# Optimization experiments

Hardware: AMD Instinct MI355X
Metric: run time of the kernel (lower is better)

The kernel has to match this reference:

```python
import jax, jax.numpy as jnp
import numpy as np

D_MODEL = 2048
N_HEADS = 16
D_HEAD = D_MODEL // N_HEADS
SQLEN = 2048
EPS = 1e-5
XPOS_SCALE_BASE = 512.0


def apply_xpos(x, offset, inv=False):
    # x: (sqlen, d_head). Rotary embedding with xPos exponential length scaling.
    sqlen, d = x.shape
    half = d // 2
    freq = 1.0 / (10000.0 ** (jnp.arange(half, dtype=jnp.float32) / half))
    pos = jnp.arange(sqlen, dtype=jnp.float32) + offset  # absolute positions
    ang = pos[:, None] * freq[None, :]                   # (sqlen, half)
    sin, cos = jnp.sin(ang), jnp.cos(ang)
    # xPos per-dim scale zeta^(pos/scale_base); k gets the inverse scale.
    zeta = (jnp.arange(half, dtype=jnp.float32) * 2.0 + 0.4 * d) / (1.4 * d)
    sc = zeta[None, :] ** (pos[:, None] / XPOS_SCALE_BASE)
    if inv:
        sc = 1.0 / sc
    x1, x2 = x[:, :half], x[:, half:]
    r1 = (x1 * cos - x2 * sin) * sc
    r2 = (x2 * cos + x1 * sin) * sc
    return jnp.concatenate([r1, r2], axis=-1)


def group_norm(x, weight, bias):
    # x: (sqlen, d_model); n_heads groups of d_head channels each.
    xg = x.reshape(x.shape[0], N_HEADS, D_HEAD)
    mu = jnp.mean(xg, axis=-1, keepdims=True)
    var = jnp.mean((xg - mu) ** 2, axis=-1, keepdims=True)
    xn = ((xg - mu) * jax.lax.rsqrt(var + EPS)).reshape(x.shape)
    return xn * weight + bias


def setup_inputs() -> dict:
    key = jax.random.key(0)
    ks = jax.random.split(key, 9)
    s = 0.02
    return {
        "x": jax.random.normal(ks[0], (SQLEN, D_MODEL), dtype=jnp.float32),
        "state": jax.random.normal(ks[1], (N_HEADS, D_HEAD, D_HEAD), dtype=jnp.float32),
        "W_qkv": jax.random.normal(ks[2], (3 * D_MODEL, D_MODEL), dtype=jnp.float32) * s,
        "W_alpha": jax.random.normal(ks[3], (N_HEADS, D_MODEL), dtype=jnp.float32) * s,
        "b_alpha": jnp.zeros((N_HEADS,), dtype=jnp.float32),
        "alpha_base": jnp.log(jax.random.uniform(ks[4], (N_HEADS,), minval=0.95, maxval=0.999)).astype(jnp.float32),
        "gn_weight": jnp.ones((D_MODEL,), dtype=jnp.float32),
        "gn_bias": jnp.zeros((D_MODEL,), dtype=jnp.float32),
        "W_out": jax.random.normal(ks[5], (D_MODEL, D_MODEL), dtype=jnp.float32) * s,
        "W_gate": jax.random.normal(ks[6], (D_MODEL, D_MODEL), dtype=jnp.float32) * s,
        "offset": 0,
    }


def reference(x, state, W_qkv, W_alpha, b_alpha, alpha_base, gn_weight, gn_bias, W_out, W_gate, offset):
    sqlen = x.shape[0]
    # qkv projection -> (3, h, sqlen, d_head)
    qkv = (x @ W_qkv.T).reshape(sqlen, 3, N_HEADS, D_HEAD).transpose(1, 2, 0, 3)
    q, k, v = qkv[0], qkv[1], qkv[2]
    q = jax.vmap(lambda t: apply_xpos(t, offset))(q)
    k = jax.vmap(lambda t: apply_xpos(t, offset, inv=True))(k)

    # per-head, per-position decay log-rates: (h, sqlen), negative
    alphas = jax.nn.sigmoid(x @ W_alpha.T + b_alpha).T
    alphas = alpha_base[:, None] * 8.0 * alphas
    k = (1.0 - jnp.exp(alphas))[:, :, None] * k
    alphas = jnp.cumsum(alphas, axis=1)
    # causal decay matrix Delta[h,i,j] = exp(a_i - a_j) for j <= i
    Delta = jnp.tril(jnp.exp(alphas[:, :, None] - alphas[:, None, :]))

    attn = jnp.einsum('hid,hjd,hij->hij', q, k, Delta)
    ret = jnp.einsum('hij,hje->ihe', attn, v)  # (sqlen, h, d_head)

    # recurrent state carry
    new_state = jnp.exp(alphas[:, -1, None, None]) * state
    ret = ret + jnp.einsum('hid,hde,hi->ihe', q, state, jnp.exp(alphas))
    new_state = new_state + jnp.einsum('hid,hie,hi->hde', k, v, Delta[:, -1, :])

    ret = ret.reshape(sqlen, D_MODEL)
    ret = group_norm(ret, gn_weight, gn_bias)
    out = (jax.nn.swish(ret @ W_gate.T) * ret) @ W_out.T
    return (out, new_state)
```

## Files before the change

### kernel.cpp

```cpp
#include <hip/hip_runtime.h>
#include <cstddef>

#define SQLEN 2048
#define DMODEL 2048
#define NHEADS 16
#define DHEAD 128

typedef __attribute__((ext_vector_type(8))) short bf16x8;
typedef __attribute__((ext_vector_type(4))) float floatx4;

__device__ __forceinline__ unsigned short f2bf(float f) {
  union { float f; unsigned u; } c; c.f = f;
  unsigned u = c.u;
  unsigned r = u + 0x7fffu + ((u >> 16) & 1u);
  return (unsigned short)(r >> 16);
}
__device__ __forceinline__ float bf2f(unsigned short s) {
  union { unsigned u; float f; } c; c.u = ((unsigned)s) << 16;
  return c.f;
}

__global__ __launch_bounds__(256) void f2b_kernel(const float4* __restrict__ in,
                                                  ushort4* __restrict__ out) {
  int i = blockIdx.x * 256 + threadIdx.x;
  float4 v = in[i];
  ushort4 o;
  o.x = f2bf(v.x); o.y = f2bf(v.y); o.z = f2bf(v.z); o.w = f2bf(v.w);
  out[i] = o;
}

__global__ __launch_bounds__(256) void f2b2_kernel(const float4* __restrict__ in0,
                                                   ushort4* __restrict__ out0,
                                                   const float4* __restrict__ in1,
                                                   ushort4* __restrict__ out1,
                                                   int half_blocks) {
  int b = blockIdx.x;
  const float4* in = (b < half_blocks) ? in0 : in1;
  ushort4* out = (b < half_blocks) ? out0 : out1;
  int i = (b < half_blocks ? b : b - half_blocks) * 256 + threadIdx.x;
  float4 v = in[i];
  ushort4 o;
  o.x = f2bf(v.x); o.y = f2bf(v.y); o.z = f2bf(v.z); o.w = f2bf(v.w);
  out[i] = o;
}

__global__ __launch_bounds__(256) void gemm_bf16_nt(const unsigned short* __restrict__ A,
                                                    const unsigned short* __restrict__ B,
                                                    float* __restrict__ C,
                                                    int M, int N, int K) {
  __shared__ __align__(16) unsigned short As[128 * 32];
  __shared__ __align__(16) unsigned short Bs[128 * 32];
  int tid = threadIdx.x;
  int wave = tid >> 6;
  int lane = tid & 63;
  int wm = wave >> 1, wn = wave & 1;
  int quad = lane >> 4, m16 = lane & 15;
  int row0 = blockIdx.y * 128, col0 = blockIdx.x * 128;

  floatx4 acc[4][4];
#pragma unroll
  for (int i = 0; i < 4; i++)
#pragma unroll
    for (int j = 0; j < 4; j++) acc[i][j] = (floatx4){0.f, 0.f, 0.f, 0.f};

  int c0 = tid, c1 = tid + 256;
  int r0c = c0 >> 2, q0c = (c0 & 3) * 8;
  int r1c = c1 >> 2, q1c = (c1 & 3) * 8;

  const size_t sK = (size_t)K;
  for (int k0 = 0; k0 < K; k0 += 32) {
    __builtin_amdgcn_global_load_lds(
        (const __attribute__((address_space(1))) unsigned int*)(A + (size_t)(row0 + r0c) * sK + k0 + q0c),
        (__attribute__((address_space(3))) unsigned int*)(As + c0 * 8), 16, 0, 0);
    __builtin_amdgcn_global_load_lds(
        (const __attribute__((address_space(1))) unsigned int*)(A + (size_t)(row0 + r1c) * sK + k0 + q1c),
        (__attribute__((address_space(3))) unsigned int*)(As + c1 * 8), 16, 0, 0);
    __builtin_amdgcn_global_load_lds(
        (const __attribute__((address_space(1))) unsigned int*)(B + (size_t)(col0 + r0c) * sK + k0 + q0c),
        (__attribute__((address_space(3))) unsigned int*)(Bs + c0 * 8), 16, 0, 0);
    __builtin_amdgcn_global_load_lds(
        (const __attribute__((address_space(1))) unsigned int*)(B + (size_t)(col0 + r1c) * sK + k0 + q1c),
        (__attribute__((address_space(3))) unsigned int*)(Bs + c1 * 8), 16, 0, 0);
    __syncthreads();

    bf16x8 af[4], bfr[4];
#pragma unroll
    for (int i = 0; i < 4; i++)
      af[i] = *(const bf16x8*)(As + (wm * 64 + i * 16 + m16) * 32 + quad * 8);
#pragma unroll
    for (int j = 0; j < 4; j++)
      bfr[j] = *(const bf16x8*)(Bs + (wn * 64 + j * 16 + m16) * 32 + quad * 8);
#pragma unroll
    for (int i = 0; i < 4; i++)
#pragma unroll
      for (int j = 0; j < 4; j++)
        acc[i][j] = __builtin_amdgcn_mfma_f32_16x16x32_bf16(af[i], bfr[j], acc[i][j], 0, 0, 0);
    __syncthreads();
  }

#pragma unroll
  for (int i = 0; i < 4; i++) {
#pragma unroll
    for (int j = 0; j < 4; j++) {
      int rr = row0 + wm * 64 + i * 16 + quad * 4;
      int cc = col0 + wn * 64 + j * 16 + m16;
#pragma unroll
      for (int r = 0; r < 4; r++)
        C[(size_t)(rr + r) * N + cc] = acc[i][j][r];
    }
  }
}

__global__ __launch_bounds__(256) void gemm_swish_nt(const unsigned short* __restrict__ A,
                                                     const unsigned short* __restrict__ B,
                                                     const float* __restrict__ rn,
                                                     unsigned short* __restrict__ Hb,
                                                     int M, int N, int K) {
  __shared__ __align__(16) unsigned short As[128 * 32];
  __shared__ __align__(16) unsigned short Bs[128 * 32];
  int tid = threadIdx.x;
  int wave = tid >> 6;
  int lane = tid & 63;
  int wm = wave >> 1, wn = wave & 1;
  int quad = lane >> 4, m16 = lane & 15;
  int row0 = blockIdx.y * 128, col0 = blockIdx.x * 128;

  floatx4 acc[4][4];
#pragma unroll
  for (int i = 0; i < 4; i++)
#pragma unroll
    for (int j = 0; j < 4; j++) acc[i][j] = (floatx4){0.f, 0.f, 0.f, 0.f};

  int c0 = tid, c1 = tid + 256;
  int r0c = c0 >> 2, q0c = (c0 & 3) * 8;
  int r1c = c1 >> 2, q1c = (c1 & 3) * 8;

  const size_t sK = (size_t)K;
  for (int k0 = 0; k0 < K; k0 += 32) {
    __builtin_amdgcn_global_load_lds(
        (const __attribute__((address_space(1))) unsigned int*)(A + (size_t)(row0 + r0c) * sK + k0 + q0c),
        (__attribute__((address_space(3))) unsigned int*)(As + c0 * 8), 16, 0, 0);
    __builtin_amdgcn_global_load_lds(
        (const __attribute__((address_space(1))) unsigned int*)(A + (size_t)(row0 + r1c) * sK + k0 + q1c),
        (__attribute__((address_space(3))) unsigned int*)(As + c1 * 8), 16, 0, 0);
    __builtin_amdgcn_global_load_lds(
        (const __attribute__((address_space(1))) unsigned int*)(B + (size_t)(col0 + r0c) * sK + k0 + q0c),
        (__attribute__((address_space(3))) unsigned int*)(Bs + c0 * 8), 16, 0, 0);
    __builtin_amdgcn_global_load_lds(
        (const __attribute__((address_space(1))) unsigned int*)(B + (size_t)(col0 + r1c) * sK + k0 + q1c),
        (__attribute__((address_space(3))) unsigned int*)(Bs + c1 * 8), 16, 0, 0);
    __syncthreads();

    bf16x8 af[4], bfr[4];
#pragma unroll
    for (int i = 0; i < 4; i++)
      af[i] = *(const bf16x8*)(As + (wm * 64 + i * 16 + m16) * 32 + quad * 8);
#pragma unroll
    for (int j = 0; j < 4; j++)
      bfr[j] = *(const bf16x8*)(Bs + (wn * 64 + j * 16 + m16) * 32 + quad * 8);
#pragma unroll
    for (int i = 0; i < 4; i++)
#pragma unroll
      for (int j = 0; j < 4; j++)
        acc[i][j] = __builtin_amdgcn_mfma_f32_16x16x32_bf16(af[i], bfr[j], acc[i][j], 0, 0, 0);
    __syncthreads();
  }

#pragma unroll
  for (int i = 0; i < 4; i++) {
#pragma unroll
    for (int j = 0; j < 4; j++) {
      int rr = row0 + wm * 64 + i * 16 + quad * 4;
      int cc = col0 + wn * 64 + j * 16 + m16;
#pragma unroll
      for (int r = 0; r < 4; r++) {
        float g = acc[i][j][r];
        float rv = rn[(size_t)(rr + r) * N + cc];
        float hh = g / (1.f + __expf(-g)) * rv;
        Hb[(size_t)(rr + r) * N + cc] = f2bf(hh);
      }
    }
  }
}

__global__ __launch_bounds__(256) void alpha_kernel(const float* __restrict__ x,
                                                    const float* __restrict__ W_alpha,
                                                    const float* __restrict__ b_alpha,
                                                    const float* __restrict__ alpha_base,
                                                    float* __restrict__ a_raw) {
  __shared__ float xs[4][2048];
  int tid = threadIdx.x;
  int t0 = blockIdx.x * 4;
#pragma unroll
  for (int p = 0; p < 8; p++) {
    int idx = tid + p * 256;
    int row = idx >> 9, c4 = idx & 511;
    *(float4*)&xs[row][c4 * 4] = *(const float4*)(x + (size_t)(t0 + row) * DMODEL + c4 * 4);
  }
  __syncthreads();
  int w = tid >> 6, lane = tid & 63;
  int t = t0 + w;
#pragma unroll
  for (int h = 0; h < NHEADS; h++) {
    const float4* wr = (const float4*)(W_alpha + (size_t)h * DMODEL);
    float s = 0.f;
#pragma unroll
    for (int i = lane; i < 512; i += 64) {
      float4 a = *(const float4*)&xs[w][i * 4];
      float4 b = wr[i];
      s += a.x * b.x + a.y * b.y + a.z * b.z + a.w * b.w;
    }
#pragma unroll
    for (int off = 32; off > 0; off >>= 1) s += __shfl_down(s, off);
    if (lane == 0) {
      float sig = 1.f / (1.f + __expf(-(s + b_alpha[h])));
      a_raw[(size_t)h * SQLEN + t] = alpha_base[h] * 8.f * sig;
    }
  }
}

__global__ __launch_bounds__(256) void cumsum_kernel(const float* __restrict__ a_raw,
                                                     float* __restrict__ A) {
  int h = blockIdx.x;
  __shared__ float part[256];
  int tid = threadIdx.x;
  float v[8];
  float s = 0.f;
#pragma unroll
  for (int i = 0; i < 8; i++) {
    v[i] = a_raw[(size_t)h * SQLEN + tid * 8 + i];
    s += v[i];
  }
  part[tid] = s;
  __syncthreads();
  for (int off = 1; off < 256; off <<= 1) {
    float tmp = (tid >= off) ? part[tid - off] : 0.f;
    __syncthreads();
    part[tid] += tmp;
    __syncthreads();
  }
  float run = (tid > 0) ? part[tid - 1] : 0.f;
#pragma unroll
  for (int i = 0; i < 8; i++) {
    run += v[i];
    A[(size_t)h * SQLEN + tid * 8 + i] = run;
  }
}

__global__ __launch_bounds__(256) void xpos_kernel(const float* __restrict__ qkv,
                                                   const float* __restrict__ a_raw,
                                                   const int* __restrict__ offset_p,
                                                   unsigned short* __restrict__ qb,
                                                   unsigned short* __restrict__ kb,
                                                   unsigned short* __restrict__ vb) {
  int idx = blockIdx.x * 256 + threadIdx.x;
  int j = idx & 63;
  int t = (idx >> 6) & 2047;
  int h = idx >> 17;
  float pos = (float)(t + offset_p[0]);
  float freq = exp2f(-(float)j * (13.287712379549449f / 64.f));
  float ang = pos * freq;
  float sn = __sinf(ang), cs = __cosf(ang);
  float zeta = (2.f * (float)j + 51.2f) / 179.2f;
  float lzp = __log2f(zeta) * pos * (1.f / 512.f);
  float sc = exp2f(lzp);
  float sci = exp2f(-lzp);
  const float* row = qkv + (size_t)t * (3 * DMODEL);
  int base = h * DHEAD + j;
  float q1 = row[base], q2 = row[base + 64];
  float k1 = row[DMODEL + base], k2 = row[DMODEL + base + 64];
  float v1 = row[2 * DMODEL + base], v2 = row[2 * DMODEL + base + 64];
  size_t o = ((size_t)h * SQLEN + t) * DHEAD + j;
  qb[o] = f2bf((q1 * cs - q2 * sn) * sc);
  qb[o + 64] = f2bf((q2 * cs + q1 * sn) * sc);
  float km = (1.f - __expf(a_raw[(size_t)h * SQLEN + t])) * sci;
  kb[o] = f2bf((k1 * cs - k2 * sn) * km);
  kb[o + 64] = f2bf((k2 * cs + k1 * sn) * km);
  vb[o] = f2bf(v1);
  vb[o + 64] = f2bf(v2);
}

__global__ __launch_bounds__(256) void transpose_kv_kernel(const unsigned short* __restrict__ kb,
                                                           const unsigned short* __restrict__ vb,
                                                           const float* __restrict__ A,
                                                           unsigned short* __restrict__ kT,
                                                           unsigned short* __restrict__ vT) {
  __shared__ __align__(16) unsigned short tile[64][72];
  int h = blockIdx.z >> 1, sel = blockIdx.z & 1;
  int t0 = blockIdx.x * 64, d0 = blockIdx.y * 64;
  int tid = threadIdx.x;
  const unsigned short* src = (sel ? vb : kb) + ((size_t)h * SQLEN + t0) * DHEAD + d0;
  unsigned short* dst = (sel ? vT : kT) + (size_t)h * (DHEAD * SQLEN) + (size_t)d0 * SQLEN + t0;
  float B = A[(size_t)h * SQLEN + SQLEN - 1];
#pragma unroll
  for (int p = 0; p < 2; p++) {
    int c = tid + p * 256;
    int r = c >> 3, off = (c & 7) * 8;
    bf16x8 in = *(const bf16x8*)(src + (size_t)r * DHEAD + off);
    if (!sel) {
      float w = __expf(B - A[(size_t)h * SQLEN + t0 + r]);
      bf16x8 o;
#pragma unroll
      for (int j = 0; j < 8; j++) o[j] = (short)f2bf(bf2f((unsigned short)in[j]) * w);
      *(bf16x8*)&tile[r][off] = o;
    } else {
      *(bf16x8*)&tile[r][off] = in;
    }
  }
  __syncthreads();
#pragma unroll
  for (int p = 0; p < 2; p++) {
    int c = tid + p * 256;
    int dr = c >> 3, toff = (c & 7) * 8;
    bf16x8 o;
#pragma unroll
    for (int j = 0; j < 8; j++) o[j] = (short)tile[toff + j][dr];
    *(bf16x8*)(dst + (size_t)dr * SQLEN + toff) = o;
  }
}

__global__ __launch_bounds__(256) void transpose_state_kernel(const float* __restrict__ st,
                                                              unsigned short* __restrict__ stT) {
  __shared__ float tile[64][65];
  int h = blockIdx.z, d0 = blockIdx.x * 64, e0 = blockIdx.y * 64;
  int tid = threadIdx.x;
  const float* src = st + (size_t)h * 16384 + (size_t)d0 * DHEAD + e0;
#pragma unroll
  for (int p = 0; p < 4; p++) {
    int idx = tid + p * 256;
    int r = idx >> 4, c = (idx & 15) * 4;
    float4 f = *(const float4*)(src + (size_t)r * DHEAD + c);
    tile[r][c] = f.x; tile[r][c + 1] = f.y; tile[r][c + 2] = f.z; tile[r][c + 3] = f.w;
  }
  __syncthreads();
  unsigned short* dst = stT + (size_t)h * 16384 + (size_t)e0 * DHEAD + d0;
#pragma unroll
  for (int p = 0; p < 2; p++) {
    int idx = tid + p * 256;
    int er = idx >> 3, doff = (idx & 7) * 8;
    bf16x8 o;
#pragma unroll
    for (int j = 0; j < 8; j++) o[j] = (short)f2bf(tile[doff + j][er]);
    *(bf16x8*)(dst + (size_t)er * DHEAD + doff) = o;
  }
}

__global__ __launch_bounds__(256) void retention_mfma(const unsigned short* __restrict__ qb,
                                                      const unsigned short* __restrict__ kb,
                                                      const unsigned short* __restrict__ vT,
                                                      const unsigned short* __restrict__ stT,
                                                      const float* __restrict__ A,
                                                      const float* __restrict__ gn_w,
                                                      const float* __restrict__ gn_b,
                                                      float* __restrict__ rn,
                                                      unsigned short* __restrict__ rnb) {
  __shared__ __align__(16) unsigned short ks[64 * 128];
  __shared__ __align__(16) unsigned short vs[128 * 64];
  __shared__ __align__(16) unsigned short Ss[64 * 72];
  __shared__ float djs[64];
  int h = blockIdx.x;
  int i0 = blockIdx.y * 64;
  int tid = threadIdx.x;
  int wave = tid >> 6, lane = tid & 63, quad = lane >> 4, m16 = lane & 15;
  const float* Ah = A + (size_t)h * SQLEN;
  float c = Ah[i0];
  int rq = wave * 16 + m16;

  const unsigned short* qh = qb + ((size_t)h * SQLEN + i0 + rq) * DHEAD;
  bf16x8 qf[4];
#pragma unroll
  for (int dc = 0; dc < 4; dc++)
    qf[dc] = *(const bf16x8*)(qh + dc * 32 + quad * 8);
  float ei = __expf(Ah[i0 + rq] - c);

  float wg[8], bg[8];
#pragma unroll
  for (int et = 0; et < 8; et++) {
    int col = h * DHEAD + et * 16 + m16;
    wg[et] = gn_w[col];
    bg[et] = gn_b[col];
  }

  floatx4 acc[8];
#pragma unroll
  for (int et = 0; et < 8; et++) acc[et] = (floatx4){0.f, 0.f, 0.f, 0.f};

  if (c > -87.f) {
    const unsigned short* sp = stT + (size_t)h * 16384;
    float ecr[4];
#pragma unroll
    for (int r = 0; r < 4; r++) ecr[r] = __expf(Ah[i0 + wave * 16 + quad * 4 + r]);
#pragma unroll
    for (int et = 0; et < 8; et++) {
#pragma unroll
      for (int dc = 0; dc < 4; dc++) {
        bf16x8 sf = *(const bf16x8*)(sp + (et * 16 + m16) * DHEAD + dc * 32 + quad * 8);
        acc[et] = __builtin_amdgcn_mfma_f32_16x16x32_bf16(qf[dc], sf, acc[et], 0, 0, 0);
      }
#pragma unroll
      for (int r = 0; r < 4; r++) acc[et][r] *= ecr[r];
    }
  }

  for (int j0 = 0; j0 <= i0; j0 += 64) {
    if (c - Ah[j0 + 63] < -87.f) continue;
    __syncthreads();
    const unsigned short* kh = kb + ((size_t)h * SQLEN + j0) * DHEAD;
    const unsigned short* vh = vT + (size_t)h * (DHEAD * SQLEN) + j0;
#pragma unroll
    for (int p = 0; p < 4; p++) {
      int cch = tid + p * 256;
      int r = cch >> 4, kp = (cch & 15) ^ (r & 7);
      __builtin_amdgcn_global_load_lds(
          (const __attribute__((address_space(1))) unsigned int*)(kh + (size_t)r * DHEAD + kp * 8),
          (__attribute__((address_space(3))) unsigned int*)(ks + cch * 8), 16, 0, 0);
      int e = cch >> 3, tp = (cch & 7) ^ (e & 7);
      __builtin_amdgcn_global_load_lds(
          (const __attribute__((address_space(1))) unsigned int*)(vh + (size_t)e * SQLEN + tp * 8),
          (__attribute__((address_space(3))) unsigned int*)(vs + cch * 8), 16, 0, 0);
    }
    if (tid < 64) djs[tid] = __expf(c - Ah[j0 + tid]);
    __syncthreads();

    bool diag = (j0 == i0);
#pragma unroll
    for (int jt = 0; jt < 4; jt++) {
      floatx4 s = (floatx4){0.f, 0.f, 0.f, 0.f};
#pragma unroll
      for (int dc = 0; dc < 4; dc++) {
        int rk = jt * 16 + m16;
        bf16x8 kf = *(const bf16x8*)(ks + rk * 128 + (((dc * 4 + quad) ^ (rk & 7)) * 8));
        s = __builtin_amdgcn_mfma_f32_16x16x32_bf16(kf, qf[dc], s, 0, 0, 0);
      }
      int jb = jt * 16 + quad * 4;
      float4 dj4 = *(const float4*)&djs[jb];
      ushort4 pk;
      pk.x = f2bf((diag && (jb + 0 > rq)) ? 0.f : s[0] * ei * dj4.x);
      pk.y = f2bf((diag && (jb + 1 > rq)) ? 0.f : s[1] * ei * dj4.y);
      pk.z = f2bf((diag && (jb + 2 > rq)) ? 0.f : s[2] * ei * dj4.z);
      pk.w = f2bf((diag && (jb + 3 > rq)) ? 0.f : s[3] * ei * dj4.w);
      *(ushort4*)(Ss + rq * 72 + jb) = pk;
    }

    bf16x8 sfr[2];
#pragma unroll
    for (int kc = 0; kc < 2; kc++)
      sfr[kc] = *(const bf16x8*)(Ss + rq * 72 + kc * 32 + quad * 8);
#pragma unroll
    for (int et = 0; et < 8; et++) {
#pragma unroll
      for (int kc = 0; kc < 2; kc++) {
        int e = et * 16 + m16;
        bf16x8 vf = *(const bf16x8*)(vs + e * 64 + (((kc * 4 + quad) ^ (e & 7)) * 8));
        acc[et] = __builtin_amdgcn_mfma_f32_16x16x32_bf16(sfr[kc], vf, acc[et], 0, 0, 0);
      }
    }
  }

#pragma unroll
  for (int r = 0; r < 4; r++) {
    float s = 0.f, ss = 0.f;
#pragma unroll
    for (int et = 0; et < 8; et++) {
      float v = acc[et][r];
      s += v; ss += v * v;
    }
#pragma unroll
    for (int off = 8; off > 0; off >>= 1) {
      s += __shfl_xor(s, off);
      ss += __shfl_xor(ss, off);
    }
    float mu = s * (1.f / 128.f);
    float var = ss * (1.f / 128.f) - mu * mu;
    float inv = rsqrtf(var + 1e-5f);
    int row = i0 + wave * 16 + quad * 4 + r;
    size_t o = (size_t)row * DMODEL + h * DHEAD;
#pragma unroll
    for (int et = 0; et < 8; et++) {
      float rv = (acc[et][r] - mu) * inv * wg[et] + bg[et];
      rn[o + et * 16 + m16] = rv;
      rnb[o + et * 16 + m16] = f2bf(rv);
    }
  }
}

__global__ __launch_bounds__(256) void state_gemm(const unsigned short* __restrict__ kT,
                                                  const unsigned short* __restrict__ vT,
                                                  float* __restrict__ P) {
  __shared__ __align__(16) unsigned short As[128 * 32];
  __shared__ __align__(16) unsigned short Bs[128 * 32];
  int chunk = blockIdx.x, h = blockIdx.y;
  int tid = threadIdx.x;
  int wave = tid >> 6, lane = tid & 63;
  int wm = wave >> 1, wn = wave & 1;
  int quad = lane >> 4, m16 = lane & 15;
  const unsigned short* Ab = kT + (size_t)h * (DHEAD * SQLEN);
  const unsigned short* Bb = vT + (size_t)h * (DHEAD * SQLEN);

  floatx4 acc[4][4];
#pragma unroll
  for (int i = 0; i < 4; i++)
#pragma unroll
    for (int j = 0; j < 4; j++) acc[i][j] = (floatx4){0.f, 0.f, 0.f, 0.f};

  int c0 = tid, c1 = tid + 256;
  int r0c = c0 >> 2, q0c = (c0 & 3) * 8;
  int r1c = c1 >> 2, q1c = (c1 & 3) * 8;

  for (int k0 = chunk * 256; k0 < chunk * 256 + 256; k0 += 32) {
    __builtin_amdgcn_global_load_lds(
        (const __attribute__((address_space(1))) unsigned int*)(Ab + (size_t)r0c * SQLEN + k0 + q0c),
        (__attribute__((address_space(3))) unsigned int*)(As + c0 * 8), 16, 0, 0);
    __builtin_amdgcn_global_load_lds(
        (const __attribute__((address_space(1))) unsigned int*)(Ab + (size_t)r1c * SQLEN + k0 + q1c),
        (__attribute__((address_space(3))) unsigned int*)(As + c1 * 8), 16, 0, 0);
    __builtin_amdgcn_global_load_lds(
        (const __attribute__((address_space(1))) unsigned int*)(Bb + (size_t)r0c * SQLEN + k0 + q0c),
        (__attribute__((address_space(3))) unsigned int*)(Bs + c0 * 8), 16, 0, 0);
    __builtin_amdgcn_global_load_lds(
        (const __attribute__((address_space(1))) unsigned int*)(Bb + (size_t)r1c * SQLEN + k0 + q1c),
        (__attribute__((address_space(3))) unsigned int*)(Bs + c1 * 8), 16, 0, 0);
    __syncthreads();

    bf16x8 af[4], bfr[4];
#pragma unroll
    for (int i = 0; i < 4; i++)
      af[i] = *(const bf16x8*)(As + (wm * 64 + i * 16 + m16) * 32 + quad * 8);
#pragma unroll
    for (int j = 0; j < 4; j++)
      bfr[j] = *(const bf16x8*)(Bs + (wn * 64 + j * 16 + m16) * 32 + quad * 8);
#pragma unroll
    for (int i = 0; i < 4; i++)
#pragma unroll
      for (int j = 0; j < 4; j++)
        acc[i][j] = __builtin_amdgcn_mfma_f32_16x16x32_bf16(af[i], bfr[j], acc[i][j], 0, 0, 0);
    __syncthreads();
  }

  float* Pp = P + (size_t)(h * 8 + chunk) * 16384;
#pragma unroll
  for (int i = 0; i < 4; i++)
#pragma unroll
    for (int j = 0; j < 4; j++) {
      int rr = wm * 64 + i * 16 + quad * 4;
      int cc = wn * 64 + j * 16 + m16;
#pragma unroll
      for (int r = 0; r < 4; r++)
        Pp[(size_t)(rr + r) * DHEAD + cc] = acc[i][j][r];
    }
}

__global__ __launch_bounds__(256) void state_combine(const float* __restrict__ P,
                                                     const float* __restrict__ state,
                                                     const float* __restrict__ A,
                                                     float* __restrict__ out_state) {
  int idx = blockIdx.x * 256 + threadIdx.x;
  int h = idx >> 14;
  int de = idx & 16383;
  float B = A[(size_t)h * SQLEN + SQLEN - 1];
  float s = __expf(B) * state[idx];
#pragma unroll
  for (int c = 0; c < 8; c++) s += P[(size_t)(h * 8 + c) * 16384 + de];
  out_state[idx] = s;
}

extern "C" void kernel_launch(void* const* d_in, const int* in_sizes, int n_in,
                              void* d_out, int out_size, void* d_ws, size_t ws_size,
                              hipStream_t stream) {
  const float* x = (const float*)d_in[0];
  const float* state = (const float*)d_in[1];
  const float* W_qkv = (const float*)d_in[2];
  const float* W_alpha = (const float*)d_in[3];
  const float* b_alpha = (const float*)d_in[4];
  const float* alpha_base = (const float*)d_in[5];
  const float* gn_w = (const float*)d_in[6];
  const float* gn_b = (const float*)d_in[7];
  const float* W_out = (const float*)d_in[8];
  const float* W_gate = (const float*)d_in[9];
  const int* offset = (const int*)d_in[10];

  float* ws = (float*)d_ws;
  float* qkv = ws;
  float* P   = ws + 4194304;
  float* rn  = ws + 29360128;
  float* araw = ws + 33554432;
  float* Acum = ws + 33587200;

  unsigned short* xb    = (unsigned short*)(ws + 12582912);
  unsigned short* Wqkvb = (unsigned short*)(ws + 16777216);
  unsigned short* qb    = (unsigned short*)(ws + 12582912);
  unsigned short* kb    = (unsigned short*)(ws + 14680064);
  unsigned short* vb    = (unsigned short*)(ws + 16777216);
  unsigned short* kT_s  = (unsigned short*)(ws + 18874368);
  unsigned short* vT_b  = (unsigned short*)(ws + 20971520);
  unsigned short* stT_b = (unsigned short*)(ws + 23068672);
  unsigned short* rnb   = (unsigned short*)(ws + 25165824);
  unsigned short* Wgateb = (unsigned short*)(ws + 14680064);
  unsigned short* Woutb  = (unsigned short*)(ws + 16777216);
  unsigned short* Hb     = (unsigned short*)(ws + 18874368);

  float* out = (float*)d_out;
  float* out_state = out + 4194304;

  dim3 blk(256);
  f2b_kernel<<<dim3(4096), blk, 0, stream>>>((const float4*)x, (ushort4*)xb);
  f2b_kernel<<<dim3(12288), blk, 0, stream>>>((const float4*)W_qkv, (ushort4*)Wqkvb);
  gemm_bf16_nt<<<dim3(48, 16), blk, 0, stream>>>(xb, Wqkvb, qkv, 2048, 6144, 2048);

  alpha_kernel<<<dim3(512), blk, 0, stream>>>(x, W_alpha, b_alpha, alpha_base, araw);
  cumsum_kernel<<<dim3(16), blk, 0, stream>>>(araw, Acum);
  xpos_kernel<<<dim3(8192), blk, 0, stream>>>(qkv, araw, offset, qb, kb, vb);
  transpose_kv_kernel<<<dim3(32, 2, 32), blk, 0, stream>>>(kb, vb, Acum, kT_s, vT_b);
  transpose_state_kernel<<<dim3(2, 2, 16), blk, 0, stream>>>(state, stT_b);

  retention_mfma<<<dim3(16, 32), blk, 0, stream>>>(qb, kb, vT_b, stT_b, Acum,
                                                   gn_w, gn_b, rn, rnb);
  state_gemm<<<dim3(8, 16), blk, 0, stream>>>(kT_s, vT_b, P);
  state_combine<<<dim3(1024), blk, 0, stream>>>(P, state, Acum, out_state);

  f2b2_kernel<<<dim3(8192), blk, 0, stream>>>((const float4*)W_gate, (ushort4*)Wgateb,
                                              (const float4*)W_out, (ushort4*)Woutb, 4096);
  gemm_swish_nt<<<dim3(16, 16), blk, 0, stream>>>(rnb, Wgateb, rn, Hb, 2048, 2048, 2048);
  gemm_bf16_nt<<<dim3(16, 16), blk, 0, stream>>>(Hb, Woutb, out, 2048, 2048, 2048);
}
```

Measured before the change: 436.0 us.

## Fuse xPos rotary into QKV GEMM epilogue and swizzle LDS tiles

The QKV GEMM now applies the xPos rotation, the k decay factor and the bf16 conversion in its epilogue, writing q/k/v directly in per-head bf16 layout. W_qkv rows are permuted during conversion so each wave holds both rotary halves, and the fp32 qkv intermediate plus the separate xpos kernel are removed. All MFMA GEMMs also XOR-swizzle their LDS tile layout to cut bank conflicts. The epilogue is heavier, with transcendentals and scattered 2-byte stores, which could slow the GEMM tail.

```diff
diff --git a/kernel.cpp b/kernel.cpp
--- a/kernel.cpp
+++ b/kernel.cpp
@@ -44,6 +44,133 @@
   out[i] = o;
 }
 
+__global__ __launch_bounds__(256) void f2bperm_kernel(const float* __restrict__ in,
+                                                      unsigned short* __restrict__ out) {
+  int idx = blockIdx.x * 256 + threadIdx.x;
+  int n = idx >> 9, c4 = idx & 511;
+  int src;
+  if (n < 4096) {
+    int posh = n & 127;
+    int half = posh >> 6, p64 = posh & 63;
+    int j = (p64 < 32) ? (half * 32 + p64) : (half * 32 + p64 - 32 + 64);
+    src = (n & ~127) + j;
+  } else {
+    src = n;
+  }
+  float4 v = *(const float4*)(in + (size_t)src * DMODEL + c4 * 4);
+  ushort4 o;
+  o.x = f2bf(v.x); o.y = f2bf(v.y); o.z = f2bf(v.z); o.w = f2bf(v.w);
+  *(ushort4*)(out + (size_t)n * DMODEL + c4 * 4) = o;
+}
+
+#define SWZ(r, q) ((q) ^ (((r) >> 1) & 3))
+
+__global__ __launch_bounds__(256) void gemm_qkv_xpos(const unsigned short* __restrict__ A,
+                                                     const unsigned short* __restrict__ B,
+                                                     const float* __restrict__ a_raw,
+                                                     const int* __restrict__ offset_p,
+                                                     unsigned short* __restrict__ qb,
+                                                     unsigned short* __restrict__ kb,
+                                                     unsigned short* __restrict__ vb) {
+  __shared__ __align__(16) unsigned short As[128 * 32];
+  __shared__ __align__(16) unsigned short Bs[128 * 32];
+  const int K = 2048;
+  int tid = threadIdx.x;
+  int wave = tid >> 6, lane = tid & 63;
+  int wm = wave >> 1, wn = wave & 1;
+  int quad = lane >> 4, m16 = lane & 15;
+  int row0 = blockIdx.y * 128, col0 = blockIdx.x * 128;
+
+  floatx4 acc[4][4];
+#pragma unroll
+  for (int i = 0; i < 4; i++)
+#pragma unroll
+    for (int j = 0; j < 4; j++) acc[i][j] = (floatx4){0.f, 0.f, 0.f, 0.f};
+
+  int c0 = tid, c1 = tid + 256;
+  int r0c = c0 >> 2, p0c = c0 & 3;
+  int r1c = c1 >> 2, p1c = c1 & 3;
+  int q0c = SWZ(r0c, p0c) * 8, q1c = SWZ(r1c, p1c) * 8;
+
+  for (int k0 = 0; k0 < K; k0 += 32) {
+    __builtin_amdgcn_global_load_lds(
+        (const __attribute__((address_space(1))) unsigned int*)(A + (size_t)(row0 + r0c) * K + k0 + q0c),
+        (__attribute__((address_space(3))) unsigned int*)(As + c0 * 8), 16, 0, 0);
+    __builtin_amdgcn_global_load_lds(
+        (const __attribute__((address_space(1))) unsigned int*)(A + (size_t)(row0 + r1c) * K + k0 + q1c),
+        (__attribute__((address_space(3))) unsigned int*)(As + c1 * 8), 16, 0, 0);
+    __builtin_amdgcn_global_load_lds(
+        (const __attribute__((address_space(1))) unsigned int*)(B + (size_t)(col0 + r0c) * K + k0 + q0c),
+        (__attribute__((address_space(3))) unsigned int*)(Bs + c0 * 8), 16, 0, 0);
+    __builtin_amdgcn_global_load_lds(
+        (const __attribute__((address_space(1))) unsigned int*)(B + (size_t)(col0 + r1c) * K + k0 + q1c),
+        (__attribute__((address_space(3))) unsigned int*)(Bs + c1 * 8), 16, 0, 0);
+    __syncthreads();
+
+    bf16x8 af[4], bfr[4];
+#pragma unroll
+    for (int i = 0; i < 4; i++) {
+      int rr = wm * 64 + i * 16 + m16;
+      af[i] = *(const bf16x8*)(As + rr * 32 + SWZ(rr, quad) * 8);
+    }
+#pragma unroll
+    for (int j = 0; j < 4; j++) {
+      int rr = wn * 64 + j * 16 + m16;
+      bfr[j] = *(const bf16x8*)(Bs + rr * 32 + SWZ(rr, quad) * 8);
+    }
+#pragma unroll
+    for (int i = 0; i < 4; i++)
+#pragma unroll
+      for (int j = 0; j < 4; j++)
+        acc[i][j] = __builtin_amdgcn_mfma_f32_16x16x32_bf16(af[i], bfr[j], acc[i][j], 0, 0, 0);
+    __syncthreads();
+  }
+
+  int part = col0 >> 11;
+  int h = (col0 & 2047) >> 7;
+  int off = offset_p[0];
+
+  if (part == 2) {
+#pragma unroll
+    for (int i = 0; i < 4; i++)
+#pragma unroll
+      for (int jt = 0; jt < 4; jt++) {
+        int d = wn * 64 + jt * 16 + m16;
+#pragma unroll
+        for (int r = 0; r < 4; r++) {
+          int t = row0 + wm * 64 + i * 16 + quad * 4 + r;
+          vb[((size_t)h * SQLEN + t) * DHEAD + d] = f2bf(acc[i][jt][r]);
+        }
+      }
+  } else {
+    unsigned short* dst = part ? kb : qb;
+#pragma unroll
+    for (int jt = 0; jt < 2; jt++) {
+      int j = wn * 32 + jt * 16 + m16;
+      float freq = exp2f(-(float)j * (13.287712379549449f / 64.f));
+      float lz = __log2f((2.f * (float)j + 51.2f) / 179.2f);
+#pragma unroll
+      for (int i = 0; i < 4; i++) {
+#pragma unroll
+        for (int r = 0; r < 4; r++) {
+          int t = row0 + wm * 64 + i * 16 + quad * 4 + r;
+          float pos = (float)(t + off);
+          float ang = pos * freq;
+          float sn = __sinf(ang), cs = __cosf(ang);
+          float lzp = lz * pos * (1.f / 512.f);
+          float scl;
+          if (part == 0) scl = exp2f(lzp);
+          else scl = (1.f - __expf(a_raw[(size_t)h * SQLEN + t])) * exp2f(-lzp);
+          float x1 = acc[i][jt][r], x2 = acc[i][jt + 2][r];
+          size_t o = ((size_t)h * SQLEN + t) * DHEAD + j;
+          dst[o] = f2bf((x1 * cs - x2 * sn) * scl);
+          dst[o + 64] = f2bf((x2 * cs + x1 * sn) * scl);
+        }
+      }
+    }
+  }
+}
+
 __global__ __launch_bounds__(256) void gemm_bf16_nt(const unsigned short* __restrict__ A,
                                                     const unsigned short* __restrict__ B,
                                                     float* __restrict__ C,
@@ -51,8 +178,7 @@
   __shared__ __align__(16) unsigned short As[128 * 32];
   __shared__ __align__(16) unsigned short Bs[128 * 32];
   int tid = threadIdx.x;
-  int wave = tid >> 6;
-  int lane = tid & 63;
+  int wave = tid >> 6, lane = tid & 63;
   int wm = wave >> 1, wn = wave & 1;
   int quad = lane >> 4, m16 = lane & 15;
   int row0 = blockIdx.y * 128, col0 = blockIdx.x * 128;
@@ -64,8 +190,8 @@
     for (int j = 0; j < 4; j++) acc[i][j] = (floatx4){0.f, 0.f, 0.f, 0.f};
 
   int c0 = tid, c1 = tid + 256;
-  int r0c = c0 >> 2, q0c = (c0 & 3) * 8;
-  int r1c = c1 >> 2, q1c = (c1 & 3) * 8;
+  int r0c = c0 >> 2, q0c = SWZ(r0c, c0 & 3) * 8;
+  int r1c = c1 >> 2, q1c = SWZ(r1c, c1 & 3) * 8;
 
   const size_t sK = (size_t)K;
   for (int k0 = 0; k0 < K; k0 += 32) {
@@ -85,11 +211,15 @@
 
     bf16x8 af[4], bfr[4];
 #pragma unroll
-    for (int i = 0; i < 4; i++)
-      af[i] = *(const bf16x8*)(As + (wm * 64 + i * 16 + m16) * 32 + quad * 8);
-#pragma unroll
-    for (int j = 0; j < 4; j++)
-      bfr[j] = *(const bf16x8*)(Bs + (wn * 64 + j * 16 + m16) * 32 + quad * 8);
+    for (int i = 0; i < 4; i++) {
+      int rr = wm * 64 + i * 16 + m16;
+      af[i] = *(const bf16x8*)(As + rr * 32 + SWZ(rr, quad) * 8);
+    }
+#pragma unroll
+    for (int j = 0; j < 4; j++) {
+      int rr = wn * 64 + j * 16 + m16;
+      bfr[j] = *(const bf16x8*)(Bs + rr * 32 + SWZ(rr, quad) * 8);
+    }
 #pragma unroll
     for (int i = 0; i < 4; i++)
 #pragma unroll
@@ -119,8 +249,7 @@
   __shared__ __align__(16) unsigned short As[128 * 32];
   __shared__ __align__(16) unsigned short Bs[128 * 32];
   int tid = threadIdx.x;
-  int wave = tid >> 6;
-  int lane = tid & 63;
+  int wave = tid >> 6, lane = tid & 63;
   int wm = wave >> 1, wn = wave & 1;
   int quad = lane >> 4, m16 = lane & 15;
   int row0 = blockIdx.y * 128, col0 = blockIdx.x * 128;
@@ -132,8 +261,8 @@
     for (int j = 0; j < 4; j++) acc[i][j] = (floatx4){0.f, 0.f, 0.f, 0.f};
 
   int c0 = tid, c1 = tid + 256;
-  int r0c = c0 >> 2, q0c = (c0 & 3) * 8;
-  int r1c = c1 >> 2, q1c = (c1 & 3) * 8;
+  int r0c = c0 >> 2, q0c = SWZ(r0c, c0 & 3) * 8;
+  int r1c = c1 >> 2, q1c = SWZ(r1c, c1 & 3) * 8;
 
   const size_t sK = (size_t)K;
   for (int k0 = 0; k0 < K; k0 += 32) {
@@ -153,11 +282,15 @@
 
     bf16x8 af[4], bfr[4];
 #pragma unroll
-    for (int i = 0; i < 4; i++)
-      af[i] = *(const bf16x8*)(As + (wm * 64 + i * 16 + m16) * 32 + quad * 8);
-#pragma unroll
-    for (int j = 0; j < 4; j++)
-      bfr[j] = *(const bf16x8*)(Bs + (wn * 64 + j * 16 + m16) * 32 + quad * 8);
+    for (int i = 0; i < 4; i++) {
+      int rr = wm * 64 + i * 16 + m16;
+      af[i] = *(const bf16x8*)(As + rr * 32 + SWZ(rr, quad) * 8);
+    }
+#pragma unroll
+    for (int j = 0; j < 4; j++) {
+      int rr = wn * 64 + j * 16 + m16;
+      bfr[j] = *(const bf16x8*)(Bs + rr * 32 + SWZ(rr, quad) * 8);
+    }
 #pragma unroll
     for (int i = 0; i < 4; i++)
 #pragma unroll
@@ -245,39 +378,6 @@
     run += v[i];
     A[(size_t)h * SQLEN + tid * 8 + i] = run;
   }
-}
-
-__global__ __launch_bounds__(256) void xpos_kernel(const float* __restrict__ qkv,
-                                                   const float* __restrict__ a_raw,
-                                                   const int* __restrict__ offset_p,
-                                                   unsigned short* __restrict__ qb,
-                                                   unsigned short* __restrict__ kb,
-                                                   unsigned short* __restrict__ vb) {
-  int idx = blockIdx.x * 256 + threadIdx.x;
-  int j = idx & 63;
-  int t = (idx >> 6) & 2047;
-  int h = idx >> 17;
-  float pos = (float)(t + offset_p[0]);
-  float freq = exp2f(-(float)j * (13.287712379549449f / 64.f));
-  float ang = pos * freq;
-  float sn = __sinf(ang), cs = __cosf(ang);
-  float zeta = (2.f * (float)j + 51.2f) / 179.2f;
-  float lzp = __log2f(zeta) * pos * (1.f / 512.f);
-  float sc = exp2f(lzp);
-  float sci = exp2f(-lzp);
-  const float* row = qkv + (size_t)t * (3 * DMODEL);
-  int base = h * DHEAD + j;
-  float q1 = row[base], q2 = row[base + 64];
-  float k1 = row[DMODEL + base], k2 = row[DMODEL + base + 64];
-  float v1 = row[2 * DMODEL + base], v2 = row[2 * DMODEL + base + 64];
-  size_t o = ((size_t)h * SQLEN + t) * DHEAD + j;
-  qb[o] = f2bf((q1 * cs - q2 * sn) * sc);
-  qb[o + 64] = f2bf((q2 * cs + q1 * sn) * sc);
-  float km = (1.f - __expf(a_raw[(size_t)h * SQLEN + t])) * sci;
-  kb[o] = f2bf((k1 * cs - k2 * sn) * km);
-  kb[o + 64] = f2bf((k2 * cs + k1 * sn) * km);
-  vb[o] = f2bf(v1);
-  vb[o + 64] = f2bf(v2);
 }
 
 __global__ __launch_bounds__(256) void transpose_kv_kernel(const unsigned short* __restrict__ kb,
@@ -504,8 +604,8 @@
     for (int j = 0; j < 4; j++) acc[i][j] = (floatx4){0.f, 0.f, 0.f, 0.f};
 
   int c0 = tid, c1 = tid + 256;
-  int r0c = c0 >> 2, q0c = (c0 & 3) * 8;
-  int r1c = c1 >> 2, q1c = (c1 & 3) * 8;
+  int r0c = c0 >> 2, q0c = SWZ(r0c, c0 & 3) * 8;
+  int r1c = c1 >> 2, q1c = SWZ(r1c, c1 & 3) * 8;
 
   for (int k0 = chunk * 256; k0 < chunk * 256 + 256; k0 += 32) {
     __builtin_amdgcn_global_load_lds(
@@ -524,11 +624,15 @@
 
     bf16x8 af[4], bfr[4];
 #pragma unroll
-    for (int i = 0; i < 4; i++)
-      af[i] = *(const bf16x8*)(As + (wm * 64 + i * 16 + m16) * 32 + quad * 8);
-#pragma unroll
-    for (int j = 0; j < 4; j++)
-      bfr[j] = *(const bf16x8*)(Bs + (wn * 64 + j * 16 + m16) * 32 + quad * 8);
+    for (int i = 0; i < 4; i++) {
+      int rr = wm * 64 + i * 16 + m16;
+      af[i] = *(const bf16x8*)(As + rr * 32 + SWZ(rr, quad) * 8);
+    }
+#pragma unroll
+    for (int j = 0; j < 4; j++) {
+      int rr = wn * 64 + j * 16 + m16;
+      bfr[j] = *(const bf16x8*)(Bs + rr * 32 + SWZ(rr, quad) * 8);
+    }
 #pragma unroll
     for (int i = 0; i < 4; i++)
 #pragma unroll
@@ -580,21 +684,20 @@
   const int* offset = (const int*)d_in[10];
 
   float* ws = (float*)d_ws;
-  float* qkv = ws;
-  float* P   = ws + 4194304;
+  float* P   = ws;
   float* rn  = ws + 29360128;
   float* araw = ws + 33554432;
   float* Acum = ws + 33587200;
 
-  unsigned short* xb    = (unsigned short*)(ws + 12582912);
-  unsigned short* Wqkvb = (unsigned short*)(ws + 16777216);
-  unsigned short* qb    = (unsigned short*)(ws + 12582912);
-  unsigned short* kb    = (unsigned short*)(ws + 14680064);
-  unsigned short* vb    = (unsigned short*)(ws + 16777216);
-  unsigned short* kT_s  = (unsigned short*)(ws + 18874368);
-  unsigned short* vT_b  = (unsigned short*)(ws + 20971520);
-  unsigned short* stT_b = (unsigned short*)(ws + 23068672);
-  unsigned short* rnb   = (unsigned short*)(ws + 25165824);
+  unsigned short* xb     = (unsigned short*)(ws + 0);
+  unsigned short* Wqkvb  = (unsigned short*)(ws + 4194304);
+  unsigned short* qb     = (unsigned short*)(ws + 12582912);
+  unsigned short* kb     = (unsigned short*)(ws + 14680064);
+  unsigned short* vb     = (unsigned short*)(ws + 16777216);
+  unsigned short* kT_s   = (unsigned short*)(ws + 18874368);
+  unsigned short* vT_b   = (unsigned short*)(ws + 20971520);
+  unsigned short* stT_b  = (unsigned short*)(ws + 23068672);
+  unsigned short* rnb    = (unsigned short*)(ws + 25165824);
   unsigned short* Wgateb = (unsigned short*)(ws + 14680064);
   unsigned short* Woutb  = (unsigned short*)(ws + 16777216);
   unsigned short* Hb     = (unsigned short*)(ws + 18874368);
@@ -604,12 +707,12 @@
 
   dim3 blk(256);
   f2b_kernel<<<dim3(4096), blk, 0, stream>>>((const float4*)x, (ushort4*)xb);
-  f2b_kernel<<<dim3(12288), blk, 0, stream>>>((const float4*)W_qkv, (ushort4*)Wqkvb);
-  gemm_bf16_nt<<<dim3(48, 16), blk, 0, stream>>>(xb, Wqkvb, qkv, 2048, 6144, 2048);
-
+  f2bperm_kernel<<<dim3(12288), blk, 0, stream>>>(W_qkv, Wqkvb);
   alpha_kernel<<<dim3(512), blk, 0, stream>>>(x, W_alpha, b_alpha, alpha_base, araw);
   cumsum_kernel<<<dim3(16), blk, 0, stream>>>(araw, Acum);
-  xpos_kernel<<<dim3(8192), blk, 0, stream>>>(qkv, araw, offset, qb, kb, vb);
+
+  gemm_qkv_xpos<<<dim3(48, 16), blk, 0, stream>>>(xb, Wqkvb, araw, offset, qb, kb, vb);
+
   transpose_kv_kernel<<<dim3(32, 2, 32), blk, 0, stream>>>(kb, vb, Acum, kT_s, vT_b);
   transpose_state_kernel<<<dim3(2, 2, 16), blk, 0, stream>>>(state, stT_b);
 
```

Result: no change. 437.3 us (+0.3%).
